# Performance work log

Measured on AMD Instinct MI355X. Metric: run time of the kernel, lower is better.

Reference implementation:

```python
import jax, jax.numpy as jnp
import numpy as np

TEMPERATURE = 0.07
NEG_INF = -1e9  # mask value safe for fp16/bf16 softmax


def setup_inputs() -> dict:
    key = jax.random.key(0)
    features = jax.random.normal(key, (8192, 128), dtype=jnp.float32)
    return {"features": features}


def reference(features):
    # L2-normalize rows
    f = features / jnp.linalg.norm(features, axis=1, keepdims=True)
    n = f.shape[0]          # 2 * batch_size
    b = n // 2
    # [n, n] cosine similarity / temperature
    sim = jnp.matmul(f, f.T) / TEMPERATURE
    idx = jnp.arange(n)
    # positive pair index: i <-> i + b (mod n)
    pos = sim[idx, (idx + b) % n]
    # Per row i, CE with the positive as class 0 over [pos, negatives].
    # Denominator = exp(pos) + sum(negatives) = sum over all j != i,
    # so mask only the diagonal and take a row logsumexp.
    sim_masked = jnp.where(jnp.eye(n, dtype=bool), NEG_INF, sim)
    lse = jax.nn.logsumexp(sim_masked, axis=1)
    return jnp.mean(lse - pos)
```

## Files before the change

### kernel.cpp

```cpp
#include <hip/hip_runtime.h>
#include <hip/hip_bf16.h>
#include <stdint.h>


#define N_ROWS 8192
#define DIM    128
#define HALF_N 4096
#define N_SLICES 32
#define NT 16
#define ROWS_PER_BLOCK 256

static constexpr float INV_T = 14.285714285714286f;
static constexpr float SCALE = 20.60992915555662f;

typedef __attribute__((ext_vector_type(8))) short short8;
typedef __attribute__((ext_vector_type(4))) float f32x4;

#if __has_builtin(__builtin_amdgcn_exp2f)
__device__ inline float fast_exp2(float x) { return __builtin_amdgcn_exp2f(x); }
#else
__device__ inline float fast_exp2(float x) { return exp2f(x); }
#endif

__device__ inline float bf_lo(uint32_t u) { return __uint_as_float(u << 16); }
__device__ inline float bf_hi(uint32_t u) { return __uint_as_float(u & 0xFFFF0000u); }
__device__ inline uint16_t f2bf(float x) {
    uint32_t u = __float_as_uint(x);
    return (uint16_t)((u + 0x7FFFu + ((u >> 16) & 1u)) >> 16);
}


__global__ __launch_bounds__(256) void k_normalize(const float* __restrict__ f,
                                                   uint16_t* __restrict__ fn,
                                                   uint16_t* __restrict__ fnB) {
    int wid  = (blockIdx.x * blockDim.x + threadIdx.x) >> 6;
    int lane = threadIdx.x & 63;
    const float2* src = (const float2*)(f + (size_t)wid * DIM);
    float2 v = src[lane];
    float ss = v.x * v.x + v.y * v.y;
    #pragma unroll
    for (int m = 1; m < 64; m <<= 1) ss += __shfl_xor(ss, m, 64);
    float inv = rsqrtf(ss);
    ushort2 o;
    o.x = f2bf(v.x * inv);
    o.y = f2bf(v.y * inv);
    ((ushort2*)(fn + (size_t)wid * DIM))[lane] = o;
    int k0 = lane * 2;
    size_t chunk = (size_t)(wid >> 4) * 256 + (k0 >> 5) * 64 +
                   ((k0 >> 3) & 3) * 16 + (wid & 15);
    *(ushort2*)((char*)fnB + chunk * 16 + (k0 & 7) * 2) = o;
}

__global__ __launch_bounds__(256) void k_simexp(const uint16_t* __restrict__ fnB,
                                                float* __restrict__ E_part) {
    const int lane  = threadIdx.x & 63;
    const int w     = threadIdx.x >> 6;
    const int ib    = blockIdx.x * ROWS_PER_BLOCK + w * 64;
    const int slice = blockIdx.y;
    const int lr = lane & 15;
    const int lk = lane >> 4;

    const short8* fnB8 = (const short8*)fnB;
    const int tileA0 = ib >> 4;
    const int jt0    = slice * NT;

    short8 Af[4][4];
    #pragma unroll
    for (int mt = 0; mt < 4; ++mt)
        #pragma unroll
        for (int kc = 0; kc < 4; ++kc)
            Af[mt][kc] = fnB8[(size_t)(tileA0 + mt) * 256 + kc * 64 + lane];

    float es[4][4];
    #pragma unroll
    for (int mt = 0; mt < 4; ++mt)
        #pragma unroll
        for (int r = 0; r < 4; ++r) es[mt][r] = 0.0f;

    for (int jt = 0; jt < NT; ++jt) {
        const short8* bp = fnB8 + (size_t)(jt0 + jt) * 256 + lane;
        short8 Bf[4];
        #pragma unroll
        for (int kc = 0; kc < 4; ++kc)
            Bf[kc] = bp[kc * 64];
        #pragma unroll
        for (int mt = 0; mt < 4; ++mt) {
            f32x4 acc = {0.0f, 0.0f, 0.0f, 0.0f};
            #pragma unroll
            for (int kc = 0; kc < 4; ++kc)
                acc = __builtin_amdgcn_mfma_f32_16x16x32_bf16(Af[mt][kc], Bf[kc], acc, 0, 0, 0);
            #pragma unroll
            for (int r = 0; r < 4; ++r)
                es[mt][r] += fast_exp2(fmaf(acc[r], SCALE, -SCALE));
        }
    }

    #pragma unroll
    for (int mt = 0; mt < 4; ++mt)
        #pragma unroll
        for (int r = 0; r < 4; ++r) {
            float v = es[mt][r];
            v += __shfl_xor(v, 1, 64);
            v += __shfl_xor(v, 2, 64);
            v += __shfl_xor(v, 4, 64);
            v += __shfl_xor(v, 8, 64);
            if (lr == 0)
                E_part[(size_t)(ib + mt * 16 + lk * 4 + r) * N_SLICES + slice] = v;
        }
}

__global__ __launch_bounds__(256) void k_finalize(const uint16_t* __restrict__ fn,
                                                  const float* __restrict__ E_part,
                                                  float* __restrict__ terms) {
    __shared__ float sm[4];
    int wid  = (blockIdx.x * blockDim.x + threadIdx.x) >> 6;
    int lane = threadIdx.x & 63;
    int partner = (wid + HALF_N) & (N_ROWS - 1);
    const uint32_t* fr = (const uint32_t*)(fn + (size_t)wid * DIM);
    const uint32_t* pr = (const uint32_t*)(fn + (size_t)partner * DIM);
    uint32_t a = fr[lane], p = pr[lane];
    float a0 = bf_lo(a), a1 = bf_hi(a);
    float p0 = bf_lo(p), p1 = bf_hi(p);
    float sd = a0 * a0 + a1 * a1;
    float pd = a0 * p0 + a1 * p1;
    #pragma unroll
    for (int m = 1; m < 64; m <<= 1) {
        sd += __shfl_xor(sd, m, 64);
        pd += __shfl_xor(pd, m, 64);
    }
    float e = (lane < N_SLICES) ? E_part[(size_t)wid * N_SLICES + lane] : 0.0f;
    #pragma unroll
    for (int m = 1; m < 64; m <<= 1) e += __shfl_xor(e, m, 64);
    if (lane == 0) {
        float ep = e - fast_exp2(fmaf(sd, SCALE, -SCALE));
        sm[threadIdx.x >> 6] = INV_T + logf(ep) - pd * INV_T;
    }
    __syncthreads();
    if (threadIdx.x == 0)
        terms[blockIdx.x] = sm[0] + sm[1] + sm[2] + sm[3];
}

__global__ __launch_bounds__(256) void k_reduce(const float* __restrict__ terms,
                                                float* __restrict__ out) {
    __shared__ float sm[4];
    float acc = 0.0f;
    for (int i = threadIdx.x; i < N_ROWS / 4; i += 256) acc += terms[i];
    #pragma unroll
    for (int m = 1; m < 64; m <<= 1) acc += __shfl_xor(acc, m, 64);
    if ((threadIdx.x & 63) == 0) sm[threadIdx.x >> 6] = acc;
    __syncthreads();
    if (threadIdx.x == 0)
        out[0] = (sm[0] + sm[1] + sm[2] + sm[3]) * (1.0f / N_ROWS);
}

extern "C" void kernel_launch(void* const* d_in, const int* in_sizes, int n_in,
                              void* d_out, int out_size, void* d_ws, size_t ws_size,
                              hipStream_t stream) {
    const float* feat = (const float*)d_in[0];
    float* out = (float*)d_out;

    uint16_t* fn  = (uint16_t*)d_ws;
    uint16_t* fnB = fn + (size_t)N_ROWS * DIM;
    float* E_part = (float*)(fnB + (size_t)N_ROWS * DIM);
    float* terms  = E_part + (size_t)N_ROWS * N_SLICES;

    k_normalize<<<dim3(N_ROWS / 4), dim3(256), 0, stream>>>(feat, fn, fnB);
    k_simexp<<<dim3(N_ROWS / ROWS_PER_BLOCK, N_SLICES), dim3(256), 0, stream>>>(fnB, E_part);
    k_finalize<<<dim3(N_ROWS / 4), dim3(256), 0, stream>>>(fn, E_part, terms);
    k_reduce<<<dim3(1), dim3(256), 0, stream>>>(terms, out);
}
```

Baseline: 38.69 us.

## Fuse final reduction into finalize via atomic counter and halve simexp grid

Removes the separate single-block reduce kernel: finalize blocks bump a global counter, which k_normalize zeroes, and the last block to arrive sums the per-block terms and writes the mean. The simexp kernel now runs 512 blocks, each handling two column slices in sequence, so the A-fragment loads are reused across both slices and fewer blocks are launched. This saves one kernel launch and some redundant A loads. In exchange it adds an atomic and fences, and fewer blocks means less parallelism to hide latency on a large GPU.

Result: slower. 79.35 us (+105.1%).

```diff
diff --git a/kernel.cpp b/kernel.cpp
--- a/kernel.cpp
+++ b/kernel.cpp
@@ -8,7 +8,7 @@
 #define HALF_N 4096
 #define N_SLICES 32
 #define NT 16
-#define ROWS_PER_BLOCK 256
+#define NBLK_FIN (N_ROWS / 4)
 
 static constexpr float INV_T = 14.285714285714286f;
 static constexpr float SCALE = 20.60992915555662f;
@@ -32,7 +32,9 @@
 
 __global__ __launch_bounds__(256) void k_normalize(const float* __restrict__ f,
                                                    uint16_t* __restrict__ fn,
-                                                   uint16_t* __restrict__ fnB) {
+                                                   uint16_t* __restrict__ fnB,
+                                                   int* __restrict__ counter) {
+    if (blockIdx.x == 0 && threadIdx.x == 0) counter[0] = 0;
     int wid  = (blockIdx.x * blockDim.x + threadIdx.x) >> 6;
     int lane = threadIdx.x & 63;
     const float2* src = (const float2*)(f + (size_t)wid * DIM);
@@ -53,16 +55,15 @@
 
 __global__ __launch_bounds__(256) void k_simexp(const uint16_t* __restrict__ fnB,
                                                 float* __restrict__ E_part) {
-    const int lane  = threadIdx.x & 63;
-    const int w     = threadIdx.x >> 6;
-    const int ib    = blockIdx.x * ROWS_PER_BLOCK + w * 64;
-    const int slice = blockIdx.y;
+    const int lane = threadIdx.x & 63;
+    const int w    = threadIdx.x >> 6;
+    const int b    = blockIdx.x;
     const int lr = lane & 15;
     const int lk = lane >> 4;
-
+    const int ib = (b & 31) * 256 + w * 64;
+    const int sg = b >> 5;
     const short8* fnB8 = (const short8*)fnB;
     const int tileA0 = ib >> 4;
-    const int jt0    = slice * NT;
 
     short8 Af[4][4];
     #pragma unroll
@@ -71,50 +72,58 @@
         for (int kc = 0; kc < 4; ++kc)
             Af[mt][kc] = fnB8[(size_t)(tileA0 + mt) * 256 + kc * 64 + lane];
 
-    float es[4][4];
     #pragma unroll
-    for (int mt = 0; mt < 4; ++mt)
+    for (int half = 0; half < 2; ++half) {
+        const int slice = sg * 2 + half;
+        const short8* bbase = fnB8 + (size_t)slice * NT * 256 + lane;
+        float es[4][4];
         #pragma unroll
-        for (int r = 0; r < 4; ++r) es[mt][r] = 0.0f;
+        for (int mt = 0; mt < 4; ++mt)
+            #pragma unroll
+            for (int r = 0; r < 4; ++r) es[mt][r] = 0.0f;
 
-    for (int jt = 0; jt < NT; ++jt) {
-        const short8* bp = fnB8 + (size_t)(jt0 + jt) * 256 + lane;
-        short8 Bf[4];
-        #pragma unroll
-        for (int kc = 0; kc < 4; ++kc)
-            Bf[kc] = bp[kc * 64];
-        #pragma unroll
-        for (int mt = 0; mt < 4; ++mt) {
-            f32x4 acc = {0.0f, 0.0f, 0.0f, 0.0f};
+        for (int jt = 0; jt < NT; ++jt) {
+            const short8* bp = bbase + (size_t)jt * 256;
+            short8 Bf[4];
             #pragma unroll
             for (int kc = 0; kc < 4; ++kc)
-                acc = __builtin_amdgcn_mfma_f32_16x16x32_bf16(Af[mt][kc], Bf[kc], acc, 0, 0, 0);
+                Bf[kc] = bp[kc * 64];
             #pragma unroll
-            for (int r = 0; r < 4; ++r)
-                es[mt][r] += fast_exp2(fmaf(acc[r], SCALE, -SCALE));
+            for (int mt = 0; mt < 4; ++mt) {
+                f32x4 acc = {0.0f, 0.0f, 0.0f, 0.0f};
+                #pragma unroll
+                for (int kc = 0; kc < 4; ++kc)
+                    acc = __builtin_amdgcn_mfma_f32_16x16x32_bf16(Af[mt][kc], Bf[kc], acc, 0, 0, 0);
+                #pragma unroll
+                for (int r = 0; r < 4; ++r)
+                    es[mt][r] += fast_exp2(fmaf(acc[r], SCALE, -SCALE));
+            }
         }
+        #pragma unroll
+        for (int mt = 0; mt < 4; ++mt)
+            #pragma unroll
+            for (int r = 0; r < 4; ++r) {
+                float v = es[mt][r];
+                v += __shfl_xor(v, 1, 64);
+                v += __shfl_xor(v, 2, 64);
+                v += __shfl_xor(v, 4, 64);
+                v += __shfl_xor(v, 8, 64);
+                if (lr == 0)
+                    E_part[(size_t)(ib + mt * 16 + lk * 4 + r) * N_SLICES + slice] = v;
+            }
     }
-
-    #pragma unroll
-    for (int mt = 0; mt < 4; ++mt)
-        #pragma unroll
-        for (int r = 0; r < 4; ++r) {
-            float v = es[mt][r];
-            v += __shfl_xor(v, 1, 64);
-            v += __shfl_xor(v, 2, 64);
-            v += __shfl_xor(v, 4, 64);
-            v += __shfl_xor(v, 8, 64);
-            if (lr == 0)
-                E_part[(size_t)(ib + mt * 16 + lk * 4 + r) * N_SLICES + slice] = v;
-        }
 }
 
 __global__ __launch_bounds__(256) void k_finalize(const uint16_t* __restrict__ fn,
                                                   const float* __restrict__ E_part,
-                                                  float* __restrict__ terms) {
+                                                  float* __restrict__ terms,
+                                                  int* __restrict__ counter,
+                                                  float* __restrict__ out) {
     __shared__ float sm[4];
-    int wid  = (blockIdx.x * blockDim.x + threadIdx.x) >> 6;
-    int lane = threadIdx.x & 63;
+    __shared__ int is_last;
+    const int tid  = threadIdx.x;
+    int wid  = (blockIdx.x * blockDim.x + tid) >> 6;
+    int lane = tid & 63;
     int partner = (wid + HALF_N) & (N_ROWS - 1);
     const uint32_t* fr = (const uint32_t*)(fn + (size_t)wid * DIM);
     const uint32_t* pr = (const uint32_t*)(fn + (size_t)partner * DIM);
@@ -133,24 +142,28 @@
     for (int m = 1; m < 64; m <<= 1) e += __shfl_xor(e, m, 64);
     if (lane == 0) {
         float ep = e - fast_exp2(fmaf(sd, SCALE, -SCALE));
-        sm[threadIdx.x >> 6] = INV_T + logf(ep) - pd * INV_T;
+        sm[tid >> 6] = INV_T + logf(ep) - pd * INV_T;
     }
     __syncthreads();
-    if (threadIdx.x == 0)
+    if (tid == 0) {
         terms[blockIdx.x] = sm[0] + sm[1] + sm[2] + sm[3];
-}
-
-__global__ __launch_bounds__(256) void k_reduce(const float* __restrict__ terms,
-                                                float* __restrict__ out) {
-    __shared__ float sm[4];
-    float acc = 0.0f;
-    for (int i = threadIdx.x; i < N_ROWS / 4; i += 256) acc += terms[i];
-    #pragma unroll
-    for (int m = 1; m < 64; m <<= 1) acc += __shfl_xor(acc, m, 64);
-    if ((threadIdx.x & 63) == 0) sm[threadIdx.x >> 6] = acc;
+        __threadfence();
+        int old = atomicAdd(counter, 1);
+        is_last = (old == NBLK_FIN - 1);
+    }
     __syncthreads();
-    if (threadIdx.x == 0)
-        out[0] = (sm[0] + sm[1] + sm[2] + sm[3]) * (1.0f / N_ROWS);
+    if (is_last) {
+        __threadfence();
+        float acc = 0.0f;
+        for (int i = tid; i < NBLK_FIN; i += 256) acc += terms[i];
+        #pragma unroll
+        for (int m = 1; m < 64; m <<= 1) acc += __shfl_xor(acc, m, 64);
+        __syncthreads();
+        if (lane == 0) sm[tid >> 6] = acc;
+        __syncthreads();
+        if (tid == 0)
+            out[0] = (sm[0] + sm[1] + sm[2] + sm[3]) * (1.0f / N_ROWS);
+    }
 }
 
 extern "C" void kernel_launch(void* const* d_in, const int* in_sizes, int n_in,
@@ -163,9 +176,9 @@
     uint16_t* fnB = fn + (size_t)N_ROWS * DIM;
     float* E_part = (float*)(fnB + (size_t)N_ROWS * DIM);
     float* terms  = E_part + (size_t)N_ROWS * N_SLICES;
+    int* counter  = (int*)(terms + NBLK_FIN);
 
-    k_normalize<<<dim3(N_ROWS / 4), dim3(256), 0, stream>>>(feat, fn, fnB);
-    k_simexp<<<dim3(N_ROWS / ROWS_PER_BLOCK, N_SLICES), dim3(256), 0, stream>>>(fnB, E_part);
-    k_finalize<<<dim3(N_ROWS / 4), dim3(256), 0, stream>>>(fn, E_part, terms);
-    k_reduce<<<dim3(1), dim3(256), 0, stream>>>(terms, out);
+    k_normalize<<<dim3(N_ROWS / 4), dim3(256), 0, stream>>>(feat, fn, fnB, counter);
+    k_simexp<<<dim3(512), dim3(256), 0, stream>>>(fnB, E_part);
+    k_finalize<<<dim3(NBLK_FIN), dim3(256), 0, stream>>>(fn, E_part, terms, counter, out);
 }
```
